# Performance work log

Hardware: AMD Instinct MI355X
Metric: run time of the kernel (lower is better)

The kernel has to match this reference:

```python
import jax, jax.numpy as jnp
import numpy as np

DIM = 4096
X_H_SCALE = 1.0
HAD_SCALE = 1.0 / np.sqrt(DIM)  # orthonormal FWHT normalization


def fwht(x):
    """Fast Walsh-Hadamard transform along the last axis (Sylvester order).
    x: [..., N] with N a power of 2. O(N log N) butterfly, fully vectorized
    over all leading dims; the loop is over the fixed log2(N) stages only.
    """
    n = x.shape[-1]
    stages = int(np.log2(n))
    assert 1 << stages == n, "last dim must be a power of 2"
    lead = x.shape[:-1]
    for i in range(stages):
        blk = 1 << i  # block size doubling each stage
        y = x.reshape(lead + (n // (2 * blk), 2, blk))
        a = y[..., 0, :]
        b = y[..., 1, :]
        x = jnp.concatenate([a + b, a - b], axis=-1).reshape(lead + (n,))
    return x


def setup_inputs() -> dict:
    key = jax.random.key(0)
    x = jax.random.normal(key, (4, 2048, DIM), dtype=jnp.float32)
    return {"x": x}


def reference(x):
    # forward: qx = FWHT(x) * (had_scale / x_H_scale)
    scale = jnp.asarray(HAD_SCALE / X_H_SCALE, dtype=x.dtype)
    return fwht(x) * scale
```

## Files before the change

kernel.cpp:

```cpp
#include <hip/hip_runtime.h>

#define DIM 4096
#define HAD_SCALE 0.015625f

template <int CTRL>
__device__ __forceinline__ float qperm(float v) {
    return __int_as_float(
        __builtin_amdgcn_mov_dpp(__float_as_int(v), CTRL, 0xF, 0xF, false));
}

template <int OFS>
__device__ __forceinline__ float lswz(float v) {
    return __int_as_float(
        __builtin_amdgcn_ds_swizzle(__float_as_int(v), OFS));
}

struct Signs { float sA, sB, sC, sD, sE, sF; };


__device__ __forceinline__ void loadRow(const float4* __restrict__ x4,
                                        int lane, float r[64]) {
#pragma unroll
    for (int g = 0; g < 16; g++) {
        float4 v = x4[g * 64 + lane];
        r[4 * g + 0] = v.x;
        r[4 * g + 1] = v.y;
        r[4 * g + 2] = v.z;
        r[4 * g + 3] = v.w;
    }
}

__device__ __forceinline__ void computeRow(float r[64], const Signs& s) {
#pragma unroll
    for (int g = 0; g < 16; g++) {
        {
            float a = r[4 * g + 0], b = r[4 * g + 1];
            float c = r[4 * g + 2], d = r[4 * g + 3];
            float ab0 = a + b, ab1 = a - b;
            float cd0 = c + d, cd1 = c - d;
            r[4 * g + 0] = ab0 + cd0;
            r[4 * g + 1] = ab1 + cd1;
            r[4 * g + 2] = ab0 - cd0;
            r[4 * g + 3] = ab1 - cd1;
        }
#pragma unroll
        for (int e = 0; e < 4; e++) {
            float v = r[4 * g + e];
            v = __builtin_fmaf(v, s.sA, qperm<0xB1>(v));
            v = __builtin_fmaf(v, s.sB, qperm<0x4E>(v));
            v = __builtin_fmaf(v, s.sC, lswz<0x101F>(v));
            v = __builtin_fmaf(v, s.sD, lswz<0x201F>(v));
            v = __builtin_fmaf(v, s.sE, lswz<0x401F>(v));
            v = __builtin_fmaf(v, s.sF, __shfl_xor(v, 32, 64));
            r[4 * g + e] = v;
        }
    }
#pragma unroll
    for (int st = 4; st < 64; st <<= 1) {
#pragma unroll
        for (int i = 0; i < 64; i++) {
            if ((i & st) == 0) {
                float a = r[i];
                float b = r[i ^ st];
                r[i]      = a + b;
                r[i ^ st] = a - b;
            }
        }
    }
}

__device__ __forceinline__ void storeRow(float4* __restrict__ y4,
                                         int lane, const float r[64]) {
#pragma unroll
    for (int g = 0; g < 16; g++)
        y4[g * 64 + lane] = make_float4(r[4 * g + 0] * HAD_SCALE,
                                        r[4 * g + 1] * HAD_SCALE,
                                        r[4 * g + 2] * HAD_SCALE,
                                        r[4 * g + 3] * HAD_SCALE);
}

__global__ __launch_bounds__(256) void fwht_kernel(const float* __restrict__ x,
                                                   float* __restrict__ y,
                                                   int nwaves) {
    const int t = threadIdx.x;
    const int lane = t & 63;
    const int wid = blockIdx.x * 4 + (t >> 6);

    const size_t rowA = (size_t)wid;
    const size_t rowB = (size_t)wid + (size_t)nwaves;
    const float4* __restrict__ xA = (const float4*)(x + rowA * DIM);
    const float4* __restrict__ xB = (const float4*)(x + rowB * DIM);
    float4* __restrict__ yA = (float4*)(y + rowA * DIM);
    float4* __restrict__ yB = (float4*)(y + rowB * DIM);

    Signs s;
    s.sA = (lane & 1)  ? -1.f : 1.f;
    s.sB = (lane & 2)  ? -1.f : 1.f;
    s.sC = (lane & 4)  ? -1.f : 1.f;
    s.sD = (lane & 8)  ? -1.f : 1.f;
    s.sE = (lane & 16) ? -1.f : 1.f;
    s.sF = (lane & 32) ? -1.f : 1.f;

    float rA[64], rB[64];
    loadRow(xA, lane, rA);
    loadRow(xB, lane, rB);
    computeRow(rA, s);
    storeRow(yA, lane, rA);
    computeRow(rB, s);
    storeRow(yB, lane, rB);
}

extern "C" void kernel_launch(void* const* d_in, const int* in_sizes, int n_in,
                              void* d_out, int out_size, void* d_ws, size_t ws_size,
                              hipStream_t stream) {
    const float* x = (const float*)d_in[0];
    float* y = (float*)d_out;
    const int n = in_sizes[0];
    const int rows = n / DIM;
    const int nwaves = rows / 2;
    fwht_kernel<<<nwaves / 4, 256, 0, stream>>>(x, y, nwaves);
}
```

Measured before the change: 234.0 us.

## Process four rows per wave with software-pipelined loads and nontemporal stores

Each wave now handles four rows instead of two. Loads of the next row are issued before computing the current one, with sched_barriers keeping that order, so memory latency overlaps the butterfly compute. Output stores use nontemporal hints so the write stream does not pollute the cache. In exchange, register pressure rises with up to three 64-float row buffers live at once, and the grid shrinks to half as many waves, which may reduce occupancy and parallelism.

```diff
diff --git a/kernel.cpp b/kernel.cpp
--- a/kernel.cpp
+++ b/kernel.cpp
@@ -2,6 +2,8 @@
 
 #define DIM 4096
 #define HAD_SCALE 0.015625f
+
+typedef float floatx4 __attribute__((ext_vector_type(4)));
 
 template <int CTRL>
 __device__ __forceinline__ float qperm(float v) {
@@ -69,14 +71,17 @@
     }
 }
 
-__device__ __forceinline__ void storeRow(float4* __restrict__ y4,
-                                         int lane, const float r[64]) {
+__device__ __forceinline__ void storeRowNT(floatx4* __restrict__ y4,
+                                           int lane, const float r[64]) {
 #pragma unroll
-    for (int g = 0; g < 16; g++)
-        y4[g * 64 + lane] = make_float4(r[4 * g + 0] * HAD_SCALE,
-                                        r[4 * g + 1] * HAD_SCALE,
-                                        r[4 * g + 2] * HAD_SCALE,
-                                        r[4 * g + 3] * HAD_SCALE);
+    for (int g = 0; g < 16; g++) {
+        floatx4 v;
+        v.x = r[4 * g + 0] * HAD_SCALE;
+        v.y = r[4 * g + 1] * HAD_SCALE;
+        v.z = r[4 * g + 2] * HAD_SCALE;
+        v.w = r[4 * g + 3] * HAD_SCALE;
+        __builtin_nontemporal_store(v, &y4[g * 64 + lane]);
+    }
 }
 
 __global__ __launch_bounds__(256) void fwht_kernel(const float* __restrict__ x,
@@ -86,12 +91,9 @@
     const int lane = t & 63;
     const int wid = blockIdx.x * 4 + (t >> 6);
 
-    const size_t rowA = (size_t)wid;
-    const size_t rowB = (size_t)wid + (size_t)nwaves;
-    const float4* __restrict__ xA = (const float4*)(x + rowA * DIM);
-    const float4* __restrict__ xB = (const float4*)(x + rowB * DIM);
-    float4* __restrict__ yA = (float4*)(y + rowA * DIM);
-    float4* __restrict__ yB = (float4*)(y + rowB * DIM);
+    const float4* __restrict__ x0 = (const float4*)(x + (size_t)wid * DIM);
+    floatx4* __restrict__ y0 = (floatx4*)(y + (size_t)wid * DIM);
+    const size_t stride4 = (size_t)nwaves * (DIM / 4);
 
     Signs s;
     s.sA = (lane & 1)  ? -1.f : 1.f;
@@ -101,13 +103,23 @@
     s.sE = (lane & 16) ? -1.f : 1.f;
     s.sF = (lane & 32) ? -1.f : 1.f;
 
-    float rA[64], rB[64];
-    loadRow(xA, lane, rA);
-    loadRow(xB, lane, rB);
-    computeRow(rA, s);
-    storeRow(yA, lane, rA);
-    computeRow(rB, s);
-    storeRow(yB, lane, rB);
+    float A[64], B[64], C[64], D[64];
+
+    loadRow(x0, lane, A);
+    loadRow(x0 + stride4, lane, B);
+    __builtin_amdgcn_sched_barrier(0);
+    computeRow(A, s);
+    storeRowNT(y0, lane, A);
+    loadRow(x0 + 2 * stride4, lane, C);
+    __builtin_amdgcn_sched_barrier(0);
+    computeRow(B, s);
+    storeRowNT(y0 + stride4, lane, B);
+    loadRow(x0 + 3 * stride4, lane, D);
+    __builtin_amdgcn_sched_barrier(0);
+    computeRow(C, s);
+    storeRowNT(y0 + 2 * stride4, lane, C);
+    computeRow(D, s);
+    storeRowNT(y0 + 3 * stride4, lane, D);
 }
 
 extern "C" void kernel_launch(void* const* d_in, const int* in_sizes, int n_in,
@@ -117,6 +129,6 @@
     float* y = (float*)d_out;
     const int n = in_sizes[0];
     const int rows = n / DIM;
-    const int nwaves = rows / 2;
+    const int nwaves = rows / 4;
     fwht_kernel<<<nwaves / 4, 256, 0, stream>>>(x, y, nwaves);
 }
```

New measurement: 242.0 us. +3.4%, slower.
